# Kernel optimization log

Hardware: AMD Instinct MI355X
Metric: run time of the kernel (lower is better)

The kernel has to match this reference:

```python
import jax, jax.numpy as jnp
import numpy as np

N_USERS, N_ITEMS = 100000, 50000
K = 5 * 20          # multi_factor * top_k
D = 64              # embedding_dim
B = 8192
CAT = 2 * K * D     # 12800
HID = CAT // 100    # 128


def setup_inputs() -> dict:
    key = jax.random.key(0)
    ks = jax.random.split(key, 12)
    return {
        "user_idxs": jax.random.randint(ks[0], (B,), 0, N_USERS),
        "item_idxs": jax.random.randint(ks[1], (B,), 0, N_ITEMS),
        "user_idx_tensor": jax.random.randint(ks[2], (N_USERS, K), 0, N_USERS),
        "item_idx_tensor": jax.random.randint(ks[3], (N_ITEMS, K), 0, N_ITEMS),
        "user_scr_tensor": jax.random.uniform(ks[4], (N_USERS, K), dtype=jnp.float32),
        "item_scr_tensor": jax.random.uniform(ks[5], (N_ITEMS, K), dtype=jnp.float32),
        "user_emb": jax.random.normal(ks[6], (N_USERS, D), dtype=jnp.float32) * 0.1,
        "item_emb": jax.random.normal(ks[7], (N_ITEMS, D), dtype=jnp.float32) * 0.1,
        "W1": jax.random.normal(ks[8], (CAT, HID), dtype=jnp.float32) * 0.02,
        "b1": jnp.zeros((HID,), dtype=jnp.float32),
        "W2": jax.random.normal(ks[9], (HID, 1), dtype=jnp.float32) * 0.02,
        "b2": jnp.zeros((1,), dtype=jnp.float32),
    }


def _side(idxs, idx_tensor, scr_tensor, emb_table):
    neighs = idx_tensor[idxs]                 # [B, K] neighbor ids
    neigh_emb = emb_table[neighs]             # [B, K, D]
    neigh_scr = scr_tensor[neighs]            # [B, K, K]
    scored = jnp.einsum('bkj,bjd->bkd', neigh_scr, neigh_emb)  # [B, K, D]
    return scored.reshape(scored.shape[0], -1)                 # [B, K*D]


def reference(user_idxs, item_idxs, user_idx_tensor, item_idx_tensor,
              user_scr_tensor, item_scr_tensor, user_emb, item_emb,
              W1, b1, W2, b2):
    u = _side(user_idxs, user_idx_tensor, user_scr_tensor, user_emb)
    v = _side(item_idxs, item_idx_tensor, item_scr_tensor, item_emb)
    x = jnp.concatenate([u, v], axis=-1)      # [B, 2*K*D]
    h = jax.nn.relu(x @ W1 + b1)
    o = jax.nn.relu(h @ W2 + b2)
    return jax.nn.sigmoid(o).squeeze(-1)      # [B]
```

## Files before the change

### kernel.cpp

```cpp
#include <hip/hip_runtime.h>
#include <hip/hip_bf16.h>
#include <math.h>

constexpr int KN  = 100;
constexpr int DE  = 64;
constexpr int CAT = 2 * KN * DE;
constexpr int HID = 128;
constexpr int CHUNK = 4096;
constexpr int KSPLIT = 8;
constexpr int KSEG = CAT / KSPLIT;

typedef __bf16          bf16x8   __attribute__((ext_vector_type(8)));
typedef float           f32x4    __attribute__((ext_vector_type(4)));
typedef unsigned short  ushort8v __attribute__((ext_vector_type(8)));
typedef unsigned short  ushort4v __attribute__((ext_vector_type(4)));

static __device__ __forceinline__ unsigned short f2bf(float f) {
    __hip_bfloat16 h = __float2bfloat16(f);
    return *reinterpret_cast<unsigned short*>(&h);
}

static __device__ __forceinline__ bf16x8 mk_frag(ushort4v lo, ushort4v hi) {
    union { ushort8v u; bf16x8 b; } c;
    c.u = (ushort8v){ lo[0], lo[1], lo[2], lo[3], hi[0], hi[1], hi[2], hi[3] };
    return c.b;
}

__global__ __launch_bounds__(256) void cvt4(
    const float* __restrict__ a0, unsigned short* __restrict__ o0, int n0,
    const float* __restrict__ a1, unsigned short* __restrict__ o1, int n1,
    const float* __restrict__ a2, unsigned short* __restrict__ o2, int n2,
    const float* __restrict__ a3, unsigned short* __restrict__ o3, int n3)
{
    const float* in; unsigned short* out; int n4;
    switch (blockIdx.y) {
        case 0:  in = a0; out = o0; n4 = n0; break;
        case 1:  in = a1; out = o1; n4 = n1; break;
        case 2:  in = a2; out = o2; n4 = n2; break;
        default: in = a3; out = o3; n4 = n3; break;
    }
    for (int i = blockIdx.x * 256 + threadIdx.x; i < n4; i += gridDim.x * 256) {
        float4 v = ((const float4*)in)[i];
        ushort4v o = { f2bf(v.x), f2bf(v.y), f2bf(v.z), f2bf(v.w) };
        ((ushort4v*)out)[i] = o;
    }
}

__global__ __launch_bounds__(256) void prep_w1t(
    const float* __restrict__ W1, unsigned short* __restrict__ w1t)
{
    __shared__ unsigned short T[HID][72];
    const int t  = threadIdx.x;
    const int k0 = blockIdx.x * 64;

    for (int idx = t; idx < 64 * HID; idx += 256) {
        int kk = idx >> 7, n = idx & 127;
        T[n][kk] = f2bf(W1[(size_t)(k0 + kk) * HID + n]);
    }
    __syncthreads();
    for (int idx = t; idx < HID * 16; idx += 256) {
        int n = idx >> 4, c4 = idx & 15;
        *(ushort4v*)&w1t[(size_t)n * CAT + k0 + c4 * 4] =
            *(const ushort4v*)&T[n][c4 * 4];
    }
}

__global__ __launch_bounds__(256) void einsum_mfma(
    const int* __restrict__ u_idx, const int* __restrict__ i_idx,
    const int* __restrict__ u_nbt, const int* __restrict__ i_nbt,
    const unsigned short* __restrict__ u_scr, const unsigned short* __restrict__ i_scr,
    const unsigned short* __restrict__ u_emb, const unsigned short* __restrict__ i_emb,
    unsigned short* __restrict__ xb, int b0)
{
    __shared__ __align__(16) unsigned short ET[64][136];
    __shared__ int nb[KN];

    const int t    = threadIdx.x;
    const int side = blockIdx.y;
    const int b    = b0 + blockIdx.x;

    const int*            idxs = side ? i_idx : u_idx;
    const int*            nbt  = side ? i_nbt : u_nbt;
    const unsigned short* scr  = side ? i_scr : u_scr;
    const unsigned short* emb  = side ? i_emb : u_emb;

    const ushort4v z4 = {0, 0, 0, 0};

    const int center = idxs[b];
    if (t < KN) nb[t] = nbt[(size_t)center * KN + t];

    for (int idx = t; idx < 64 * 7; idx += 256) {
        int r = idx / 7, c = idx - r * 7;
        *(ushort4v*)&ET[r][100 + c * 4] = z4;
    }
    __syncthreads();

    for (int idx = t; idx < 25 * 16; idx += 256) {
        int d4 = idx / 25, j0 = idx - d4 * 25;
        ushort4v v0 = *(const ushort4v*)(emb + (size_t)nb[j0 * 4 + 0] * DE + d4 * 4);
        ushort4v v1 = *(const ushort4v*)(emb + (size_t)nb[j0 * 4 + 1] * DE + d4 * 4);
        ushort4v v2 = *(const ushort4v*)(emb + (size_t)nb[j0 * 4 + 2] * DE + d4 * 4);
        ushort4v v3 = *(const ushort4v*)(emb + (size_t)nb[j0 * 4 + 3] * DE + d4 * 4);
        ushort4v o0 = { v0[0], v1[0], v2[0], v3[0] };
        ushort4v o1 = { v0[1], v1[1], v2[1], v3[1] };
        ushort4v o2 = { v0[2], v1[2], v2[2], v3[2] };
        ushort4v o3 = { v0[3], v1[3], v2[3], v3[3] };
        *(ushort4v*)&ET[d4 * 4 + 0][j0 * 4] = o0;
        *(ushort4v*)&ET[d4 * 4 + 1][j0 * 4] = o1;
        *(ushort4v*)&ET[d4 * 4 + 2][j0 * 4] = o2;
        *(ushort4v*)&ET[d4 * 4 + 3][j0 * 4] = o3;
    }
    __syncthreads();

    const int w  = t >> 6;
    const int l  = t & 63;
    const int cl = l & 15;
    const int rg = l >> 4;

    const unsigned short* srow[7];
    #pragma unroll
    for (int mt = 0; mt < 7; ++mt) {
        int kr = mt * 16 + cl;
        if (kr > KN - 1) kr = KN - 1;
        srow[mt] = scr + (size_t)nb[kr] * KN;
    }

    f32x4 acc[7];
    #pragma unroll
    for (int m = 0; m < 7; ++m) acc[m] = (f32x4){0.f, 0.f, 0.f, 0.f};

    #pragma unroll
    for (int ks = 0; ks < 4; ++ks) {
        const int k0 = ks * 32 + rg * 8;
        bf16x8 bfrag = *(const bf16x8*)&ET[w * 16 + cl][k0];
        #pragma unroll
        for (int mt = 0; mt < 7; ++mt) {
            ushort4v lo, hi;
            if (ks < 3) {
                lo = *(const ushort4v*)(srow[mt] + k0);
                hi = *(const ushort4v*)(srow[mt] + k0 + 4);
            } else if (rg == 0) {
                lo = *(const ushort4v*)(srow[mt] + 96);
                hi = z4;
            } else {
                lo = z4; hi = z4;
            }
            bf16x8 afrag = mk_frag(lo, hi);
            acc[mt] = __builtin_amdgcn_mfma_f32_16x16x32_bf16(afrag, bfrag, acc[mt], 0, 0, 0);
        }
    }
    __syncthreads();

    unsigned short* X = &ET[0][0];
    #pragma unroll
    for (int mt = 0; mt < 7; ++mt) {
        #pragma unroll
        for (int rr = 0; rr < 4; ++rr) {
            int k = mt * 16 + rg * 4 + rr;
            if (k < KN) X[k * 72 + w * 16 + cl] = f2bf(acc[mt][rr]);
        }
    }
    __syncthreads();

    unsigned short* xr = xb + (size_t)blockIdx.x * CAT + side * (KN * DE);
    for (int idx = t; idx < KN * 8; idx += 256) {
        int r = idx >> 3, c8 = idx & 7;
        __builtin_nontemporal_store(*(const ushort8v*)&X[r * 72 + c8 * 8],
                                    (ushort8v*)&xr[r * DE + c8 * 8]);
    }
}

__global__ __launch_bounds__(256) void mlp_kpart(
    const unsigned short* __restrict__ xb, const unsigned short* __restrict__ w1t,
    float* __restrict__ hp, int rows)
{
    __shared__ unsigned short A[2][64][72];
    __shared__ unsigned short Bt[2][HID][72];

    const int t  = threadIdx.x;
    const int w  = t >> 6;
    const int l  = t & 63;
    const int cl = l & 15;
    const int rg = l >> 4;
    const int row0  = blockIdx.x * 64;
    const int q     = blockIdx.y;
    const int kbase = q * KSEG;

    auto stage = [&](int buf, int kb) {
        #pragma unroll
        for (int i = 0; i < 2; ++i) {
            int c = t + i * 256;
            int r = c >> 3, c8 = c & 7;
            *(ushort8v*)&A[buf][r][c8 * 8] = __builtin_nontemporal_load(
                (const ushort8v*)&xb[(size_t)(row0 + r) * CAT + kbase + kb + c8 * 8]);
        }
        #pragma unroll
        for (int i = 0; i < 4; ++i) {
            int c = t + i * 256;
            int n = c >> 3, c8 = c & 7;
            *(ushort8v*)&Bt[buf][n][c8 * 8] =
                *(const ushort8v*)&w1t[(size_t)n * CAT + kbase + kb + c8 * 8];
        }
    };

    f32x4 acc[4][2];
    #pragma unroll
    for (int mt = 0; mt < 4; ++mt)
        #pragma unroll
        for (int nt = 0; nt < 2; ++nt)
            acc[mt][nt] = (f32x4){0.f, 0.f, 0.f, 0.f};

    stage(0, 0);
    __syncthreads();

    constexpr int NS = KSEG / 64;
    for (int s = 0; s < NS; ++s) {
        const int cur = s & 1;
        if (s + 1 < NS) stage(cur ^ 1, (s + 1) * 64);
        #pragma unroll
        for (int ks = 0; ks < 2; ++ks) {
            const int kcol = ks * 32 + rg * 8;
            bf16x8 bv0 = *(const bf16x8*)&Bt[cur][w * 32 + cl][kcol];
            bf16x8 bv1 = *(const bf16x8*)&Bt[cur][w * 32 + 16 + cl][kcol];
            #pragma unroll
            for (int mt = 0; mt < 4; ++mt) {
                bf16x8 a = *(const bf16x8*)&A[cur][mt * 16 + cl][kcol];
                acc[mt][0] = __builtin_amdgcn_mfma_f32_16x16x32_bf16(a, bv0, acc[mt][0], 0, 0, 0);
                acc[mt][1] = __builtin_amdgcn_mfma_f32_16x16x32_bf16(a, bv1, acc[mt][1], 0, 0, 0);
            }
        }
        __syncthreads();
    }

    #pragma unroll
    for (int mt = 0; mt < 4; ++mt) {
        #pragma unroll
        for (int nt = 0; nt < 2; ++nt) {
            #pragma unroll
            for (int r = 0; r < 4; ++r) {
                size_t row = (size_t)row0 + mt * 16 + rg * 4 + r;
                __builtin_nontemporal_store(acc[mt][nt][r],
                    &hp[((size_t)q * rows + row) * HID + w * 32 + nt * 16 + cl]);
            }
        }
    }
}

__global__ __launch_bounds__(256) void combine_sig(
    const float* __restrict__ hp, const float* __restrict__ b1,
    const float* __restrict__ W2, const float* __restrict__ b2,
    float* __restrict__ out, int rows)
{
    __shared__ float red[4];
    const int t    = threadIdx.x;
    const int w    = t >> 6;
    const int l    = t & 63;
    const int rsel = w >> 1;
    const int col  = (w & 1) * 64 + l;
    const size_t row = (size_t)blockIdx.x * 2 + rsel;
    const size_t qs  = (size_t)rows * HID;

    const float* hpr = hp + row * HID + col;
    float v = b1[col];
    #pragma unroll
    for (int j = 0; j < KSPLIT; ++j)
        v += __builtin_nontemporal_load(hpr + j * qs);
    float p = fmaxf(v, 0.f) * W2[col];
    p += __shfl_xor(p, 1,  64);
    p += __shfl_xor(p, 2,  64);
    p += __shfl_xor(p, 4,  64);
    p += __shfl_xor(p, 8,  64);
    p += __shfl_xor(p, 16, 64);
    p += __shfl_xor(p, 32, 64);
    if (l == 0) red[w] = p;
    __syncthreads();
    if (t < 2) {
        float o = red[2 * t] + red[2 * t + 1] + b2[0];
        o = fmaxf(o, 0.f);
        out[blockIdx.x * 2 + t] = 1.f / (1.f + expf(-o));
    }
}

extern "C" void kernel_launch(void* const* d_in, const int* in_sizes, int n_in,
                              void* d_out, int out_size, void* d_ws, size_t ws_size,
                              hipStream_t stream)
{
    const int*   user_idxs = (const int*)d_in[0];
    const int*   item_idxs = (const int*)d_in[1];
    const int*   user_nbt  = (const int*)d_in[2];
    const int*   item_nbt  = (const int*)d_in[3];
    const float* user_scr  = (const float*)d_in[4];
    const float* item_scr  = (const float*)d_in[5];
    const float* user_emb  = (const float*)d_in[6];
    const float* item_emb  = (const float*)d_in[7];
    const float* W1        = (const float*)d_in[8];
    const float* b1        = (const float*)d_in[9];
    const float* W2        = (const float*)d_in[10];
    const float* b2        = (const float*)d_in[11];
    float*       out       = (float*)d_out;

    const int B = in_sizes[0];

    char* p = (char*)d_ws;
    unsigned short* w1t   = (unsigned short*)p;  p += (size_t)HID * CAT * 2;
    unsigned short* us_bf = (unsigned short*)p;  p += (size_t)in_sizes[4] * 2;
    unsigned short* is_bf = (unsigned short*)p;  p += (size_t)in_sizes[5] * 2;
    unsigned short* ue_bf = (unsigned short*)p;  p += (size_t)in_sizes[6] * 2;
    unsigned short* ie_bf = (unsigned short*)p;  p += (size_t)in_sizes[7] * 2;
    float*          hpb   = (float*)p;           p += (size_t)KSPLIT * CHUNK * HID * 4;
    unsigned short* xb    = (unsigned short*)p;

    prep_w1t<<<CAT / 64, 256, 0, stream>>>(W1, w1t);
    cvt4<<<dim3(512, 4), 256, 0, stream>>>(
        user_scr, us_bf, in_sizes[4] / 4,
        item_scr, is_bf, in_sizes[5] / 4,
        user_emb, ue_bf, in_sizes[6] / 4,
        item_emb, ie_bf, in_sizes[7] / 4);

    for (int b0 = 0; b0 < B; b0 += CHUNK) {
        int rows = (B - b0 < CHUNK) ? (B - b0) : CHUNK;
        einsum_mfma<<<dim3(rows, 2), 256, 0, stream>>>(
            user_idxs, item_idxs, user_nbt, item_nbt,
            us_bf, is_bf, ue_bf, ie_bf, xb, b0);
        mlp_kpart<<<dim3(rows / 64, KSPLIT), 256, 0, stream>>>(
            xb, w1t, hpb, rows);
        combine_sig<<<rows / 2, 256, 0, stream>>>(
            hpb, b1, W2, b2, out + b0, rows);
    }
}
```

Measured before the change: 312.2 us.

## Software-pipeline einsum, MLP and combine stages across chunks in one fused launch

Replaces the three per-chunk kernels with a single pipe_step kernel. Each launch runs the combine for chunk k-2, the K-split MLP for chunk k-1 and the gather/einsum for chunk k, picking the role from the block index. The x and partial-hidden buffers are double-buffered so the stages can run concurrently, letting the latency-bound gathers overlap the MFMA work and cutting the number of serialized launches. The chunk size is halved and the MLP K-tile drops from 64 to 32 to shrink shared memory. The trade-off is more K-loop barriers, and the einsum blocks now carry the larger shared allocation.

```diff
diff --git a/kernel.cpp b/kernel.cpp
--- a/kernel.cpp
+++ b/kernel.cpp
@@ -6,9 +6,10 @@
 constexpr int DE  = 64;
 constexpr int CAT = 2 * KN * DE;
 constexpr int HID = 128;
-constexpr int CHUNK = 4096;
+constexpr int CHUNK = 2048;
 constexpr int KSPLIT = 8;
 constexpr int KSEG = CAT / KSPLIT;
+constexpr int MLP_BK = 32;
 
 typedef __bf16          bf16x8   __attribute__((ext_vector_type(8)));
 typedef float           f32x4    __attribute__((ext_vector_type(4)));
@@ -65,25 +66,18 @@
     }
 }
 
-__global__ __launch_bounds__(256) void einsum_mfma(
-    const int* __restrict__ u_idx, const int* __restrict__ i_idx,
-    const int* __restrict__ u_nbt, const int* __restrict__ i_nbt,
-    const unsigned short* __restrict__ u_scr, const unsigned short* __restrict__ i_scr,
-    const unsigned short* __restrict__ u_emb, const unsigned short* __restrict__ i_emb,
-    unsigned short* __restrict__ xb, int b0)
-{
-    __shared__ __align__(16) unsigned short ET[64][136];
-    __shared__ int nb[KN];
-
-    const int t    = threadIdx.x;
-    const int side = blockIdx.y;
-    const int b    = b0 + blockIdx.x;
-
-    const int*            idxs = side ? i_idx : u_idx;
-    const int*            nbt  = side ? i_nbt : u_nbt;
-    const unsigned short* scr  = side ? i_scr : u_scr;
-    const unsigned short* emb  = side ? i_emb : u_emb;
-
+
+__device__ __forceinline__ void einsum_body(
+    unsigned char* smem,
+    const int* __restrict__ idxs, const int* __restrict__ nbt,
+    const unsigned short* __restrict__ scr, const unsigned short* __restrict__ emb,
+    unsigned short* __restrict__ xr, int b)
+{
+    typedef unsigned short (*ET_t)[136];
+    ET_t ET = (ET_t)smem;
+    int* nb = (int*)(smem + 64 * 136 * 2);
+
+    const int t = threadIdx.x;
     const ushort4v z4 = {0, 0, 0, 0};
 
     const int center = idxs[b];
@@ -151,7 +145,7 @@
     }
     __syncthreads();
 
-    unsigned short* X = &ET[0][0];
+    unsigned short* X = (unsigned short*)smem;
     #pragma unroll
     for (int mt = 0; mt < 7; ++mt) {
         #pragma unroll
@@ -162,7 +156,6 @@
     }
     __syncthreads();
 
-    unsigned short* xr = xb + (size_t)blockIdx.x * CAT + side * (KN * DE);
     for (int idx = t; idx < KN * 8; idx += 256) {
         int r = idx >> 3, c8 = idx & 7;
         __builtin_nontemporal_store(*(const ushort8v*)&X[r * 72 + c8 * 8],
@@ -170,36 +163,38 @@
     }
 }
 
-__global__ __launch_bounds__(256) void mlp_kpart(
+__device__ __forceinline__ void mlp_body(
+    unsigned char* smem,
     const unsigned short* __restrict__ xb, const unsigned short* __restrict__ w1t,
-    float* __restrict__ hp, int rows)
-{
-    __shared__ unsigned short A[2][64][72];
-    __shared__ unsigned short Bt[2][HID][72];
+    float* __restrict__ hp, int rows, int mb, int mrb)
+{
+    typedef unsigned short (*A_t)[64][40];
+    typedef unsigned short (*B_t)[HID][40];
+    A_t A  = (A_t)smem;
+    B_t Bt = (B_t)(smem + 2 * 64 * 40 * 2);
 
     const int t  = threadIdx.x;
     const int w  = t >> 6;
     const int l  = t & 63;
     const int cl = l & 15;
     const int rg = l >> 4;
-    const int row0  = blockIdx.x * 64;
-    const int q     = blockIdx.y;
+    const int bx = mb % mrb;
+    const int q  = mb / mrb;
+    const int row0  = bx * 64;
     const int kbase = q * KSEG;
 
     auto stage = [&](int buf, int kb) {
+        {
+            int r = t >> 2, c = t & 3;
+            *(ushort8v*)&A[buf][r][c * 8] = __builtin_nontemporal_load(
+                (const ushort8v*)&xb[(size_t)(row0 + r) * CAT + kbase + kb + c * 8]);
+        }
         #pragma unroll
         for (int i = 0; i < 2; ++i) {
-            int c = t + i * 256;
-            int r = c >> 3, c8 = c & 7;
-            *(ushort8v*)&A[buf][r][c8 * 8] = __builtin_nontemporal_load(
-                (const ushort8v*)&xb[(size_t)(row0 + r) * CAT + kbase + kb + c8 * 8]);
-        }
-        #pragma unroll
-        for (int i = 0; i < 4; ++i) {
-            int c = t + i * 256;
-            int n = c >> 3, c8 = c & 7;
-            *(ushort8v*)&Bt[buf][n][c8 * 8] =
-                *(const ushort8v*)&w1t[(size_t)n * CAT + kbase + kb + c8 * 8];
+            int c2 = t + i * 256;
+            int n = c2 >> 2, c = c2 & 3;
+            *(ushort8v*)&Bt[buf][n][c * 8] =
+                *(const ushort8v*)&w1t[(size_t)n * CAT + kbase + kb + c * 8];
         }
     };
 
@@ -213,21 +208,18 @@
     stage(0, 0);
     __syncthreads();
 
-    constexpr int NS = KSEG / 64;
+    constexpr int NS = KSEG / MLP_BK;
     for (int s = 0; s < NS; ++s) {
         const int cur = s & 1;
-        if (s + 1 < NS) stage(cur ^ 1, (s + 1) * 64);
-        #pragma unroll
-        for (int ks = 0; ks < 2; ++ks) {
-            const int kcol = ks * 32 + rg * 8;
-            bf16x8 bv0 = *(const bf16x8*)&Bt[cur][w * 32 + cl][kcol];
-            bf16x8 bv1 = *(const bf16x8*)&Bt[cur][w * 32 + 16 + cl][kcol];
-            #pragma unroll
-            for (int mt = 0; mt < 4; ++mt) {
-                bf16x8 a = *(const bf16x8*)&A[cur][mt * 16 + cl][kcol];
-                acc[mt][0] = __builtin_amdgcn_mfma_f32_16x16x32_bf16(a, bv0, acc[mt][0], 0, 0, 0);
-                acc[mt][1] = __builtin_amdgcn_mfma_f32_16x16x32_bf16(a, bv1, acc[mt][1], 0, 0, 0);
-            }
+        if (s + 1 < NS) stage(cur ^ 1, (s + 1) * MLP_BK);
+        const int kcol = rg * 8;
+        bf16x8 bv0 = *(const bf16x8*)&Bt[cur][w * 32 + cl][kcol];
+        bf16x8 bv1 = *(const bf16x8*)&Bt[cur][w * 32 + 16 + cl][kcol];
+        #pragma unroll
+        for (int mt = 0; mt < 4; ++mt) {
+            bf16x8 a = *(const bf16x8*)&A[cur][mt * 16 + cl][kcol];
+            acc[mt][0] = __builtin_amdgcn_mfma_f32_16x16x32_bf16(a, bv0, acc[mt][0], 0, 0, 0);
+            acc[mt][1] = __builtin_amdgcn_mfma_f32_16x16x32_bf16(a, bv1, acc[mt][1], 0, 0, 0);
         }
         __syncthreads();
     }
@@ -246,18 +238,19 @@
     }
 }
 
-__global__ __launch_bounds__(256) void combine_sig(
+__device__ __forceinline__ void combine_body(
+    unsigned char* smem,
     const float* __restrict__ hp, const float* __restrict__ b1,
     const float* __restrict__ W2, const float* __restrict__ b2,
-    float* __restrict__ out, int rows)
-{
-    __shared__ float red[4];
+    float* __restrict__ out, int rows, int cb)
+{
+    float* red = (float*)smem;
     const int t    = threadIdx.x;
     const int w    = t >> 6;
     const int l    = t & 63;
     const int rsel = w >> 1;
     const int col  = (w & 1) * 64 + l;
-    const size_t row = (size_t)blockIdx.x * 2 + rsel;
+    const size_t row = (size_t)cb * 2 + rsel;
     const size_t qs  = (size_t)rows * HID;
 
     const float* hpr = hp + row * HID + col;
@@ -277,8 +270,42 @@
     if (t < 2) {
         float o = red[2 * t] + red[2 * t + 1] + b2[0];
         o = fmaxf(o, 0.f);
-        out[blockIdx.x * 2 + t] = 1.f / (1.f + expf(-o));
-    }
+        out[cb * 2 + t] = 1.f / (1.f + expf(-o));
+    }
+}
+
+__global__ __launch_bounds__(256) void pipe_step(
+    const int* __restrict__ u_idx, const int* __restrict__ i_idx,
+    const int* __restrict__ u_nbt, const int* __restrict__ i_nbt,
+    const unsigned short* __restrict__ u_scr, const unsigned short* __restrict__ i_scr,
+    const unsigned short* __restrict__ u_emb, const unsigned short* __restrict__ i_emb,
+    unsigned short* __restrict__ e_xb, int e_b0,
+    const unsigned short* __restrict__ m_xb, const unsigned short* __restrict__ w1t,
+    float* __restrict__ m_hp, int m_rows, int m_nblk,
+    const float* __restrict__ c_hp, const float* __restrict__ b1,
+    const float* __restrict__ W2, const float* __restrict__ b2,
+    float* __restrict__ c_out, int c_rows, int c_nblk)
+{
+    __shared__ __align__(16) unsigned char smem[2 * 64 * 40 * 2 + 2 * HID * 40 * 2];
+
+    int bid = blockIdx.x;
+    if (bid < c_nblk) {
+        combine_body(smem, c_hp, b1, W2, b2, c_out, c_rows, bid);
+        return;
+    }
+    bid -= c_nblk;
+    if (bid < m_nblk) {
+        mlp_body(smem, m_xb, w1t, m_hp, m_rows, bid, m_rows / 64);
+        return;
+    }
+    bid -= m_nblk;
+    const int row  = bid >> 1;
+    const int side = bid & 1;
+    einsum_body(smem,
+                side ? i_idx : u_idx, side ? i_nbt : u_nbt,
+                side ? i_scr : u_scr, side ? i_emb : u_emb,
+                e_xb + (size_t)row * CAT + side * (KN * DE),
+                e_b0 + row);
 }
 
 extern "C" void kernel_launch(void* const* d_in, const int* in_sizes, int n_in,
@@ -300,6 +327,7 @@
     float*       out       = (float*)d_out;
 
     const int B = in_sizes[0];
+    const int C = (B + CHUNK - 1) / CHUNK;
 
     char* p = (char*)d_ws;
     unsigned short* w1t   = (unsigned short*)p;  p += (size_t)HID * CAT * 2;
@@ -307,8 +335,12 @@
     unsigned short* is_bf = (unsigned short*)p;  p += (size_t)in_sizes[5] * 2;
     unsigned short* ue_bf = (unsigned short*)p;  p += (size_t)in_sizes[6] * 2;
     unsigned short* ie_bf = (unsigned short*)p;  p += (size_t)in_sizes[7] * 2;
-    float*          hpb   = (float*)p;           p += (size_t)KSPLIT * CHUNK * HID * 4;
-    unsigned short* xb    = (unsigned short*)p;
+    float*          hpb[2];
+    hpb[0] = (float*)p;  p += (size_t)KSPLIT * CHUNK * HID * 4;
+    hpb[1] = (float*)p;  p += (size_t)KSPLIT * CHUNK * HID * 4;
+    unsigned short* xbuf[2];
+    xbuf[0] = (unsigned short*)p;  p += (size_t)CHUNK * CAT * 2;
+    xbuf[1] = (unsigned short*)p;
 
     prep_w1t<<<CAT / 64, 256, 0, stream>>>(W1, w1t);
     cvt4<<<dim3(512, 4), 256, 0, stream>>>(
@@ -317,14 +349,26 @@
         user_emb, ue_bf, in_sizes[6] / 4,
         item_emb, ie_bf, in_sizes[7] / 4);
 
-    for (int b0 = 0; b0 < B; b0 += CHUNK) {
-        int rows = (B - b0 < CHUNK) ? (B - b0) : CHUNK;
-        einsum_mfma<<<dim3(rows, 2), 256, 0, stream>>>(
+    for (int k = 0; k <= C + 1; ++k) {
+        int e_rows = 0, m_rows = 0, c_rows = 0;
+        if (k < C) { e_rows = B - k * CHUNK; if (e_rows > CHUNK) e_rows = CHUNK; }
+        int m_c = k - 1;
+        if (m_c >= 0 && m_c < C) { m_rows = B - m_c * CHUNK; if (m_rows > CHUNK) m_rows = CHUNK; }
+        int c_c = k - 2;
+        if (c_c >= 0 && c_c < C) { c_rows = B - c_c * CHUNK; if (c_rows > CHUNK) c_rows = CHUNK; }
+
+        const int e_nblk = e_rows * 2;
+        const int m_nblk = (m_rows / 64) * KSPLIT;
+        const int c_nblk = c_rows / 2;
+        const int grid = c_nblk + m_nblk + e_nblk;
+        if (grid == 0) continue;
+
+        pipe_step<<<grid, 256, 0, stream>>>(
             user_idxs, item_idxs, user_nbt, item_nbt,
-            us_bf, is_bf, ue_bf, ie_bf, xb, b0);
-        mlp_kpart<<<dim3(rows / 64, KSPLIT), 256, 0, stream>>>(
-            xb, w1t, hpb, rows);
-        combine_sig<<<rows / 2, 256, 0, stream>>>(
-            hpb, b1, W2, b2, out + b0, rows);
-    }
-}
+            us_bf, is_bf, ue_bf, ie_bf,
+            xbuf[k & 1], k * CHUNK,
+            xbuf[(k - 1) & 1], w1t, hpb[(k - 1) & 1], m_rows, m_nblk,
+            hpb[k & 1], b1, W2, b2,
+            out + (c_c > 0 ? (size_t)c_c * CHUNK : 0), c_rows, c_nblk);
+    }
+}
```

Measured after the change: 382.3 us. 22.5% more time.
